# Kernel tuning notes

Hardware: AMD Instinct MI355X
Metric: run time of the kernel (lower is better)

## Reference

```python
import jax, jax.numpy as jnp
import numpy as np
from jax import lax

WIN_SIZE = 11
SIGMA = 1.5
CHANNELS = 3
C1 = (0.01 * 255) ** 2
C2 = (0.03 * 255) ** 2


def fspecial_gauss(size, sigma, channels):
    x, y = np.mgrid[-size // 2 + 1:size // 2 + 1, -size // 2 + 1:size // 2 + 1]
    g = np.exp(-((x ** 2 + y ** 2) / (2.0 * sigma ** 2)))
    g = (g / g.sum()).astype(np.float32)
    # depthwise kernel, OIHW with I=1, O=channels
    return jnp.asarray(np.tile(g[None, None], (channels, 1, 1, 1)))


def _gauss_filter(x, win):
    # depthwise valid conv, NCHW
    return lax.conv_general_dilated(
        x, win, window_strides=(1, 1), padding='VALID',
        feature_group_count=x.shape[1],
        dimension_numbers=('NCHW', 'OIHW', 'NCHW'))


def setup_inputs() -> dict:
    key = jax.random.key(0)
    k1, k2 = jax.random.split(key)
    X = jax.random.uniform(k1, (32, 3, 512, 512), dtype=jnp.float32)
    Y = jax.random.uniform(k2, (32, 3, 512, 512), dtype=jnp.float32)
    win = fspecial_gauss(WIN_SIZE, SIGMA, CHANNELS)
    return {"X": X, "Y": Y, "win": win}


def reference(X, Y, win):
    mu1 = _gauss_filter(X, win)
    mu2 = _gauss_filter(Y, win)
    mu1_sq = mu1 * mu1
    mu2_sq = mu2 * mu2
    mu1_mu2 = mu1 * mu2
    sigma1_sq = _gauss_filter(X * X, win) - mu1_sq
    sigma2_sq = _gauss_filter(Y * Y, win) - mu2_sq
    sigma12 = _gauss_filter(X * Y, win) - mu1_mu2
    cs_map = jax.nn.relu((2 * sigma12 + C2) / (sigma1_sq + sigma2_sq + C2))
    ssim_map = (2 * mu1_mu2 + C1) / (mu1_sq + mu2_sq + C1) * cs_map
    ssim_val = jnp.mean(ssim_map, axis=(1, 2, 3))  # per-image SSIM
    return 1.0 - jnp.mean(ssim_val)  # as_loss=True
```

## Files before the change

### kernel.cpp

```cpp
#include <hip/hip_runtime.h>
#include <math.h>


#define WIN   11
#define IMG   512
#define OUT_N 502
#define TO_R  32
#define TO_C  64
#define TI_C  (TO_C + WIN - 1)
#define VB_W  77
#define C1F   6.5025f
#define C2F   58.5225f

struct GaussW { float w[WIN]; };

__global__ __launch_bounds__(256) void ssim_v5_kernel(
    const float* __restrict__ X, const float* __restrict__ Y,
    GaussW gw, double* __restrict__ acc)
{
    __shared__ float vb[5][TO_R][VB_W];

    const int plane = blockIdx.z;
    const int ox0 = blockIdx.x * TO_C;
    const int oy0 = blockIdx.y * TO_R;
    const float* Xp = X + (size_t)plane * IMG * IMG;
    const float* Yp = Y + (size_t)plane * IMG * IMG;
    const int tid  = threadIdx.x;
    const int wave = tid >> 6;
    const int lane = tid & 63;

    {
        const int s  = wave;
        const int r0 = oy0 + s * 8;
        for (int c = lane; c < TI_C; c += 64) {
            int gc = ox0 + c; if (gc > IMG - 1) gc = IMG - 1;

            float a0[8] = {0}, a1[8] = {0}, a2[8] = {0}, a3[8] = {0}, a4[8] = {0};
#pragma unroll
            for (int k = 0; k < 18; ++k) {
                int gr = r0 + k; if (gr > IMG - 1) gr = IMG - 1;
                size_t off = (size_t)gr * IMG + gc;
                float x = Xp[off];
                float y = Yp[off];
                float xx = x * x, yy = y * y, xy = x * y;
                const int jlo = (k > 10) ? (k - 10) : 0;
                const int jhi = (k < 7) ? k : 7;
#pragma unroll
                for (int j = jlo; j <= jhi; ++j) {
                    float wv = gw.w[k - j];
                    a0[j] += wv * x;
                    a1[j] += wv * y;
                    a2[j] += wv * xx;
                    a3[j] += wv * yy;
                    a4[j] += wv * xy;
                }
            }
#pragma unroll
            for (int j = 0; j < 8; ++j) {
                int i = s * 8 + j;
                vb[0][i][c] = a0[j];
                vb[1][i][c] = a1[j];
                vb[2][i][c] = a2[j];
                vb[3][i][c] = a3[j];
                vb[4][i][c] = a4[j];
            }
        }
    }
    __syncthreads();

    const int i  = tid >> 3;
    const int c0 = (tid & 7) * 8;
    const int gi = oy0 + i;
    float m[5][8];
#pragma unroll
    for (int f = 0; f < 5; ++f) {
        float v[18];
#pragma unroll
        for (int k = 0; k < 18; ++k) v[k] = vb[f][i][c0 + k];
#pragma unroll
        for (int oc = 0; oc < 8; ++oc) {
            float s = 0.f;
#pragma unroll
            for (int k = 0; k < WIN; ++k) s += gw.w[k] * v[oc + k];
            m[f][oc] = s;
        }
    }

    float psum = 0.f;
#pragma unroll
    for (int oc = 0; oc < 8; ++oc) {
        int gj = ox0 + c0 + oc;
        if (gi < OUT_N && gj < OUT_N) {
            float m1 = m[0][oc], m2 = m[1][oc];
            float mu1s = m1 * m1, mu2s = m2 * m2, mu12 = m1 * m2;
            float sig1  = m[2][oc] - mu1s;
            float sig2  = m[3][oc] - mu2s;
            float sig12 = m[4][oc] - mu12;
            float num = (2.f * mu12 + C1F) * (2.f * sig12 + C2F);
            float den = (mu1s + mu2s + C1F) * (sig1 + sig2 + C2F);
            num = fmaxf(num, 0.f);
            psum += num * __builtin_amdgcn_rcpf(den);
        }
    }

#pragma unroll
    for (int off = 32; off > 0; off >>= 1)
        psum += __shfl_down(psum, off, 64);
    __shared__ float wsum[4];
    if ((tid & 63) == 0) wsum[tid >> 6] = psum;
    __syncthreads();
    if (tid == 0) {
        float s = wsum[0] + wsum[1] + wsum[2] + wsum[3];
        atomicAdd(acc, (double)s);
    }
}

__global__ void ssim_finalize_kernel(const double* __restrict__ acc,
                                     float* __restrict__ out)
{
    if (threadIdx.x == 0 && blockIdx.x == 0) {
        const double count = (double)96 * OUT_N * OUT_N;
        out[0] = (float)(1.0 - (*acc) / count);
    }
}

extern "C" void kernel_launch(void* const* d_in, const int* in_sizes, int n_in,
                              void* d_out, int out_size, void* d_ws, size_t ws_size,
                              hipStream_t stream) {
    (void)in_sizes; (void)n_in; (void)out_size; (void)ws_size;
    const float* X = (const float*)d_in[0];
    const float* Y = (const float*)d_in[1];
    float* out = (float*)d_out;
    double* acc = (double*)d_ws;

    hipMemsetAsync(d_ws, 0, sizeof(double), stream);

    GaussW gw;
    {
        double g[WIN], s = 0.0;
        for (int i = 0; i < WIN; ++i) {
            double d = (double)(i - 5);
            g[i] = exp(-(d * d) / (2.0 * 1.5 * 1.5));
            s += g[i];
        }
        for (int i = 0; i < WIN; ++i) gw.w[i] = (float)(g[i] / s);
    }

    dim3 grid((OUT_N + TO_C - 1) / TO_C,
              (OUT_N + TO_R - 1) / TO_R,
              96);
    ssim_v5_kernel<<<grid, 256, 0, stream>>>(X, Y, gw, acc);
    ssim_finalize_kernel<<<1, 64, 0, stream>>>(acc, out);
}
```

Measured before the change: 313.8 us.

## Merge x²+y² channel, pack filters as float2, and widen tiles

Blurs x²+y² as one quantity instead of x² and y² separately, since SSIM only needs their sum, cutting the filtered channels from five to four. Channels are packed as float2 pairs to allow packed FMA on CDNA, and the tile changes to 16x118 with a 128-wide input so each thread handles exactly one column in the vertical pass. This reduces halo redundancy horizontally but raises vertical halo overhead (26 input rows per 16 output rows), and the clamped smem column read at index TI_C touches a padding column.

```diff
diff --git a/kernel.cpp b/kernel.cpp
--- a/kernel.cpp
+++ b/kernel.cpp
@@ -5,20 +5,25 @@
 #define WIN   11
 #define IMG   512
 #define OUT_N 502
-#define TO_R  32
-#define TO_C  64
-#define TI_C  (TO_C + WIN - 1)
-#define VB_W  77
+#define TO_R  16
+#define TO_C  118
+#define TI_C  128
+#define VB_W  129
 #define C1F   6.5025f
 #define C2F   58.5225f
 
 struct GaussW { float w[WIN]; };
 
-__global__ __launch_bounds__(256) void ssim_v5_kernel(
+__device__ __forceinline__ float2 f2(float a, float b) { return make_float2(a, b); }
+__device__ __forceinline__ float2 operator+(float2 a, float2 b) { return f2(a.x+b.x, a.y+b.y); }
+__device__ __forceinline__ float2 operator*(float2 a, float2 b) { return f2(a.x*b.x, a.y*b.y); }
+
+__global__ __launch_bounds__(256) void ssim_v6_kernel(
     const float* __restrict__ X, const float* __restrict__ Y,
     GaussW gw, double* __restrict__ acc)
 {
-    __shared__ float vb[5][TO_R][VB_W];
+    __shared__ float2 vbA[TO_R][VB_W];
+    __shared__ float2 vbB[TO_R][VB_W];
 
     const int plane = blockIdx.z;
     const int ox0 = blockIdx.x * TO_C;
@@ -30,76 +35,87 @@
     const int lane = tid & 63;
 
     {
-        const int s  = wave;
+        const int s  = wave >> 1;
+        const int c  = ((wave & 1) << 6) | lane;
+        int gc = ox0 + c; if (gc > IMG - 1) gc = IMG - 1;
         const int r0 = oy0 + s * 8;
-        for (int c = lane; c < TI_C; c += 64) {
-            int gc = ox0 + c; if (gc > IMG - 1) gc = IMG - 1;
 
-            float a0[8] = {0}, a1[8] = {0}, a2[8] = {0}, a3[8] = {0}, a4[8] = {0};
+        float2 a01[8], aB[8];
 #pragma unroll
-            for (int k = 0; k < 18; ++k) {
-                int gr = r0 + k; if (gr > IMG - 1) gr = IMG - 1;
-                size_t off = (size_t)gr * IMG + gc;
-                float x = Xp[off];
-                float y = Yp[off];
-                float xx = x * x, yy = y * y, xy = x * y;
-                const int jlo = (k > 10) ? (k - 10) : 0;
-                const int jhi = (k < 7) ? k : 7;
+        for (int j = 0; j < 8; ++j) { a01[j] = f2(0.f, 0.f); aB[j] = f2(0.f, 0.f); }
+
 #pragma unroll
-                for (int j = jlo; j <= jhi; ++j) {
-                    float wv = gw.w[k - j];
-                    a0[j] += wv * x;
-                    a1[j] += wv * y;
-                    a2[j] += wv * xx;
-                    a3[j] += wv * yy;
-                    a4[j] += wv * xy;
-                }
+        for (int k = 0; k < 18; ++k) {
+            int gr = r0 + k; if (gr > IMG - 1) gr = IMG - 1;
+            size_t off = (size_t)gr * IMG + gc;
+            float x = Xp[off];
+            float y = Yp[off];
+            float2 xy  = f2(x, y);
+            float2 sq  = xy * xy;
+            float2 pb  = f2(sq.x + sq.y, x * y);
+            const int jlo = (k > 10) ? (k - 10) : 0;
+            const int jhi = (k < 7) ? k : 7;
+#pragma unroll
+            for (int j = jlo; j <= jhi; ++j) {
+                float wv = gw.w[k - j];
+                float2 wv2 = f2(wv, wv);
+                a01[j] = a01[j] + wv2 * xy;
+                aB[j]  = aB[j]  + wv2 * pb;
             }
+        }
 #pragma unroll
-            for (int j = 0; j < 8; ++j) {
-                int i = s * 8 + j;
-                vb[0][i][c] = a0[j];
-                vb[1][i][c] = a1[j];
-                vb[2][i][c] = a2[j];
-                vb[3][i][c] = a3[j];
-                vb[4][i][c] = a4[j];
-            }
+        for (int j = 0; j < 8; ++j) {
+            int i = s * 8 + j;
+            vbA[i][c] = a01[j];
+            vbB[i][c] = aB[j];
         }
     }
     __syncthreads();
 
-    const int i  = tid >> 3;
-    const int c0 = (tid & 7) * 8;
+    const int i  = tid & 15;
+    const int g  = tid >> 4;
+    const int c0 = 8 * g;
     const int gi = oy0 + i;
-    float m[5][8];
+    float psum = 0.f;
+
+    {
+        float2 v01[18], vB[18];
 #pragma unroll
-    for (int f = 0; f < 5; ++f) {
-        float v[18];
+        for (int k = 0; k < 18; ++k) {
+            int cq = c0 + k; if (cq > TI_C) cq = TI_C;
+            v01[k] = vbA[i][cq];
+            vB[k]  = vbB[i][cq];
+        }
+        float2 m01[8], mB[8];
 #pragma unroll
-        for (int k = 0; k < 18; ++k) v[k] = vb[f][i][c0 + k];
+        for (int oc = 0; oc < 8; ++oc) { m01[oc] = f2(0.f,0.f); mB[oc] = f2(0.f,0.f); }
 #pragma unroll
-        for (int oc = 0; oc < 8; ++oc) {
-            float s = 0.f;
+        for (int k = 0; k < WIN; ++k) {
+            float2 wv2 = f2(gw.w[k], gw.w[k]);
 #pragma unroll
-            for (int k = 0; k < WIN; ++k) s += gw.w[k] * v[oc + k];
-            m[f][oc] = s;
+            for (int oc = 0; oc < 8; ++oc) {
+                m01[oc] = m01[oc] + wv2 * v01[oc + k];
+                mB[oc]  = mB[oc]  + wv2 * vB[oc + k];
+            }
         }
-    }
-
-    float psum = 0.f;
+        if (gi < OUT_N) {
 #pragma unroll
-    for (int oc = 0; oc < 8; ++oc) {
-        int gj = ox0 + c0 + oc;
-        if (gi < OUT_N && gj < OUT_N) {
-            float m1 = m[0][oc], m2 = m[1][oc];
-            float mu1s = m1 * m1, mu2s = m2 * m2, mu12 = m1 * m2;
-            float sig1  = m[2][oc] - mu1s;
-            float sig2  = m[3][oc] - mu2s;
-            float sig12 = m[4][oc] - mu12;
-            float num = (2.f * mu12 + C1F) * (2.f * sig12 + C2F);
-            float den = (mu1s + mu2s + C1F) * (sig1 + sig2 + C2F);
-            num = fmaxf(num, 0.f);
-            psum += num * __builtin_amdgcn_rcpf(den);
+            for (int oc = 0; oc < 8; ++oc) {
+                int lc = c0 + oc;
+                int gj = ox0 + lc;
+                if (lc < TO_C && gj < OUT_N) {
+                    float m1 = m01[oc].x, m2 = m01[oc].y;
+                    float S  = mB[oc].x,  s12 = mB[oc].y;
+                    float mu12 = m1 * m2;
+                    float musq = m1 * m1 + m2 * m2;
+                    float sig12 = s12 - mu12;
+                    float sigsum = S - musq;
+                    float num = (2.f * mu12 + C1F) * (2.f * sig12 + C2F);
+                    float den = (musq + C1F) * (sigsum + C2F);
+                    num = fmaxf(num, 0.f);
+                    psum += num * __builtin_amdgcn_rcpf(den);
+                }
+            }
         }
     }
 
@@ -149,6 +165,6 @@
     dim3 grid((OUT_N + TO_C - 1) / TO_C,
               (OUT_N + TO_R - 1) / TO_R,
               96);
-    ssim_v5_kernel<<<grid, 256, 0, stream>>>(X, Y, gw, acc);
+    ssim_v6_kernel<<<grid, 256, 0, stream>>>(X, Y, gw, acc);
     ssim_finalize_kernel<<<1, 64, 0, stream>>>(acc, out);
 }
```

After: 346.5 us. 10.4% more time.
